# Optimization experiments

Hardware: AMD Instinct MI355X
Metric: run time of the kernel (lower is better)

Reference implementation:

```python
import jax, jax.numpy as jnp
import numpy as np

N = 10000      # nodes
E = 320000     # edges (avg degree 32)
C = 256        # feature dim (input_dim == output_dim)
L = 3          # num_layers
D = 20         # KAF dictionary size
BOUNDARY = 4.0 # KAF dictionary boundary


def setup_inputs() -> dict:
    key = jax.random.key(0)
    ks = jax.random.split(key, 7)
    x = jax.random.normal(ks[0], (N, C), jnp.float32)
    edge_index = jax.random.randint(ks[1], (2, E), 0, N, jnp.int32)
    edge_attr = jax.random.normal(ks[2], (E, 2), jnp.float32)
    # per-layer stacked parameters (all layers have identical shapes)
    node_w = jax.random.normal(ks[3], (L, C, C), jnp.float32) / jnp.sqrt(jnp.float32(C))
    edge_w = jax.random.normal(ks[4], (L, 2, C), jnp.float32) / jnp.sqrt(jnp.float32(2))
    neigh_w = jax.random.normal(ks[5], (L, C, C), jnp.float32) / jnp.sqrt(jnp.float32(C))
    bias = jnp.zeros((L, C), jnp.float32)
    alpha = jax.random.normal(ks[6], (L, C, D), jnp.float32) * 0.3
    return dict(x=x, edge_index=edge_index, edge_attr=edge_attr,
                node_w=node_w, edge_w=edge_w, neigh_w=neigh_w, bias=bias, alpha=alpha)


def _kaf(s, alpha_l):
    # Kernel Activation Function (Scardapane et al.): per-channel Gaussian mixture
    dict_pts = jnp.linspace(-BOUNDARY, BOUNDARY, D, dtype=s.dtype)  # [D]
    interval = 2.0 * BOUNDARY / (D - 1)
    gamma = 0.5 / (2.0 * interval) ** 2
    K = jnp.exp(-gamma * jnp.square(s[..., None] - dict_pts))  # [N, C, D]
    return jnp.einsum('ncd,cd->nc', K, alpha_l)


def reference(x, edge_index, edge_attr, node_w, edge_w, neigh_w, bias, alpha):
    src, dst = edge_index[0], edge_index[1]
    # mean-aggregation normalizer (computed once; graph is fixed across layers)
    cnt = jax.ops.segment_sum(jnp.ones((E,), x.dtype), dst, num_segments=N)
    inv_cnt = jnp.where(cnt > 0, 1.0 / jnp.maximum(cnt, 1.0), 0.0)  # [N]
    h = x
    for l in range(L):
        # message: edge_attr @ W_e + x_j @ W_n  -> [E, C]
        msg = edge_attr @ edge_w[l] + h[src] @ neigh_w[l]
        # mean aggregate to destination nodes
        aggr = jax.ops.segment_sum(msg, dst, num_segments=N) * inv_cnt[:, None]
        # update: KAF(aggr + x @ W + b)
        h = _kaf(aggr + h @ node_w[l] + bias[l], alpha[l])
    return h
```

## Files before the change

### kernel.cpp

```cpp
#include <hip/hip_runtime.h>
#include <hip/hip_bf16.h>

#define N_NODES 10000
#define N_EDGES 320000
#define CDIM    256
#define B_PRE   80
#define EPB     (N_EDGES / B_PRE)
#define SLK     258
#define SA      86

typedef __attribute__((ext_vector_type(8))) _Float16 half8;
typedef __attribute__((ext_vector_type(4))) _Float16 half4;
typedef __attribute__((ext_vector_type(4))) float floatx4;

#define OFF_RS    0
#define OFF_INVC  40960
#define OFF_S2    81920
#define OFF_COLV  163840
#define OFF_WCAT  806912
#define OFF_HN    1593344
#define OFF_HX    6713344
#define OFF_PERC  OFF_HN
#define OFF_BASE  (OFF_HN + 1600000)
#define OFF_EA2   OFF_HX
#define OFF_CTOT  (OFF_HX + 2560000)

__global__ __launch_bounds__(256) void k_prep(const float4* __restrict__ x, half4* __restrict__ hB,
                                              const float* __restrict__ neigh_w, const float* __restrict__ node_w,
                                              _Float16* __restrict__ wcatT) {
  __shared__ float t[32][33];
  const int b = blockIdx.x;
  if (b < 2500) {
    int i = b * 256 + threadIdx.x;
    float4 v = x[i];
    half4 h; h.x = (_Float16)v.x; h.y = (_Float16)v.y; h.z = (_Float16)v.z; h.w = (_Float16)v.w;
    hB[i] = h;
    return;
  }
  const int bb = b - 2500;
  const int k0 = (bb & 7) * 32;
  const int n0 = ((bb >> 3) & 15) * 32;
  const int l  = bb >> 7;
  const int tx = threadIdx.x & 31;
  const int ty = threadIdx.x >> 5;
  const float* src = (n0 < 256) ? neigh_w : node_w;
  const int nb = (n0 < 256) ? n0 : (n0 - 256);
#pragma unroll
  for (int p = 0; p < 4; ++p) {
    int k = k0 + ty + p * 8;
    t[ty + p * 8][tx] = src[l * 65536 + k * 256 + (nb + tx)];
  }
  __syncthreads();
#pragma unroll
  for (int p = 0; p < 4; ++p) {
    int n = n0 + ty + p * 8;
    wcatT[(size_t)l * 131072 + n * 256 + (k0 + tx)] = (_Float16)t[tx][ty + p * 8];
  }
}

__global__ __launch_bounds__(1024) void k_count(const int* __restrict__ ei,
                                                unsigned short* __restrict__ percnt) {
  __shared__ int hist[N_NODES];
  const int t = threadIdx.x, b = blockIdx.x;
  for (int n = t; n < N_NODES; n += 1024) hist[n] = 0;
  __syncthreads();
  const int e0 = b * EPB;
  for (int e = e0 + t; e < e0 + EPB; e += 1024)
    atomicAdd(&hist[ei[N_EDGES + e]], 1);
  __syncthreads();
  for (int n = t; n < N_NODES; n += 1024)
    percnt[b * N_NODES + n] = (unsigned short)hist[n];
}

__global__ __launch_bounds__(256) void k_base(const unsigned short* __restrict__ percnt,
                                              int* __restrict__ prefix, int* __restrict__ cnttot) {
  int n = blockIdx.x * 256 + threadIdx.x;
  if (n >= N_NODES) return;
  int s = 0;
  for (int b = 0; b < B_PRE; ++b) {
    prefix[b * N_NODES + n] = s;
    s += (int)percnt[b * N_NODES + n];
  }
  cnttot[n] = s;
}

__global__ __launch_bounds__(1024) void k_scan(const int* __restrict__ cnttot,
                                               int* __restrict__ rs, float* __restrict__ invc) {
  __shared__ int lds[1024];
  const int t = threadIdx.x;
  const int base = t * 10;
  int loc[10];
  int sum = 0;
#pragma unroll
  for (int i = 0; i < 10; ++i) {
    int idx = base + i;
    int v = (idx < N_NODES) ? cnttot[idx] : 0;
    loc[i] = v; sum += v;
  }
  lds[t] = sum; __syncthreads();
  for (int off = 1; off < 1024; off <<= 1) {
    int v = 0;
    if (t >= off) v = lds[t - off];
    __syncthreads();
    if (t >= off) lds[t] += v;
    __syncthreads();
  }
  int ex = lds[t] - sum;
#pragma unroll
  for (int i = 0; i < 10; ++i) {
    int idx = base + i;
    if (idx < N_NODES) {
      rs[idx] = ex; ex += loc[i];
      invc[idx] = (loc[i] > 0) ? (1.0f / (float)loc[i]) : 0.0f;
    }
  }
  if (t == 1023) rs[N_NODES] = lds[1023];
}

__global__ __launch_bounds__(1024) void k_scat(const int* __restrict__ ei, const float* __restrict__ ea,
                                               const int* __restrict__ prefix, const int* __restrict__ rs,
                                               unsigned short* __restrict__ colv, float2* __restrict__ ea2) {
  __shared__ int cur[N_NODES];
  const int t = threadIdx.x, b = blockIdx.x;
  for (int n = t; n < N_NODES; n += 1024)
    cur[n] = rs[n] + prefix[b * N_NODES + n];
  __syncthreads();
  const int e0 = b * EPB;
  for (int e = e0 + t; e < e0 + EPB; e += 1024) {
    int d = ei[N_EDGES + e];
    int src = ei[e];
    float2 a = ((const float2*)ea)[e];
    int pos = atomicAdd(&cur[d], 1);
    colv[pos] = (unsigned short)src;
    ea2[pos] = a;
  }
}

__global__ __launch_bounds__(256) void k_s2(const int* __restrict__ rs, const float2* __restrict__ ea2,
                                            float* __restrict__ s2) {
  int n = blockIdx.x * 256 + threadIdx.x;
  if (n >= N_NODES) return;
  int beg = rs[n], end = rs[n + 1];
  float sx = 0.f, sy = 0.f;
  for (int p = beg; p < end; ++p) { float2 a = ea2[p]; sx += a.x; sy += a.y; }
  s2[2 * n] = sx; s2[2 * n + 1] = sy;
}

__global__ __launch_bounds__(256) void k_gemm(const _Float16* __restrict__ A,
                                              const _Float16* __restrict__ BT,
                                              _Float16* __restrict__ hn,
                                              _Float16* __restrict__ hx) {
  __shared__ _Float16 As[64 * SLK];
  __shared__ _Float16 Bs[64 * SLK];
  const int tid = threadIdx.x;
  const int wv = tid >> 6;
  const int lane = tid & 63;
  const int m0 = blockIdx.x * 64;
  const int n0 = blockIdx.y * 64;
  const int wy = wv >> 1, wx = wv & 1;

  const int tr = tid >> 5;
  const int tc = (tid & 31) * 8;
  half8 av[8], bv[8];
#pragma unroll
  for (int s = 0; s < 8; ++s) {
    int arow = m0 + tr + 8 * s; if (arow >= N_NODES) arow = N_NODES - 1;
    av[s] = *(const half8*)(A + (size_t)arow * 256 + tc);
    bv[s] = *(const half8*)(BT + (size_t)(n0 + tr + 8 * s) * 256 + tc);
  }
#pragma unroll
  for (int s = 0; s < 8; ++s) {
    *(half8*)&As[(tr + 8 * s) * SLK + tc] = av[s];
    *(half8*)&Bs[(tr + 8 * s) * SLK + tc] = bv[s];
  }
  __syncthreads();

  floatx4 acc[2][2];
#pragma unroll
  for (int i = 0; i < 2; ++i)
#pragma unroll
    for (int j = 0; j < 2; ++j) acc[i][j] = (floatx4){0.f, 0.f, 0.f, 0.f};

  const int mrow = 32 * wy + (lane & 15);
  const int nrow = 32 * wx + (lane & 15);
  const int q8 = (lane >> 4) * 8;

#pragma unroll
  for (int kt = 0; kt < 8; ++kt) {
    const int kb = kt * 32 + q8;
    half8 af0 = *(const half8*)&As[mrow * SLK + kb];
    half8 af1 = *(const half8*)&As[(mrow + 16) * SLK + kb];
    half8 bf0 = *(const half8*)&Bs[nrow * SLK + kb];
    half8 bf1 = *(const half8*)&Bs[(nrow + 16) * SLK + kb];
    acc[0][0] = __builtin_amdgcn_mfma_f32_16x16x32_f16(af0, bf0, acc[0][0], 0, 0, 0);
    acc[0][1] = __builtin_amdgcn_mfma_f32_16x16x32_f16(af0, bf1, acc[0][1], 0, 0, 0);
    acc[1][0] = __builtin_amdgcn_mfma_f32_16x16x32_f16(af1, bf0, acc[1][0], 0, 0, 0);
    acc[1][1] = __builtin_amdgcn_mfma_f32_16x16x32_f16(af1, bf1, acc[1][1], 0, 0, 0);
  }

  const int colb = n0 + 32 * wx + (lane & 15);
  const int rowb = m0 + 32 * wy + 4 * (lane >> 4);
#pragma unroll
  for (int i = 0; i < 2; ++i) {
#pragma unroll
    for (int j = 0; j < 2; ++j) {
      const int cn = colb + 16 * j;
#pragma unroll
      for (int r = 0; r < 4; ++r) {
        const int rw = rowb + 16 * i + r;
        if (rw < N_NODES) {
          float v = acc[i][j][r];
          if (cn < 256) hn[rw * 256 + cn] = (_Float16)v;
          else          hx[rw * 256 + (cn - 256)] = (_Float16)v;
        }
      }
    }
  }
}

__global__ __launch_bounds__(256) void k_update(const int* __restrict__ rs, const unsigned short* __restrict__ colv,
                                                const float* __restrict__ invc, const float* __restrict__ s2,
                                                const _Float16* __restrict__ hn, const _Float16* __restrict__ hx,
                                                const float* __restrict__ ew,
                                                const float* __restrict__ bias,
                                                const float* __restrict__ alpha,
                                                _Float16* __restrict__ hmid, float* __restrict__ fout,
                                                int final_layer) {
  __shared__ float alds[64 * SA];
#pragma unroll
  for (int i = 0; i < 20; ++i) {
    int s = threadIdx.x + 256 * i;
    int c = s / 20, j = s - 20 * c;
    alds[(c >> 2) * SA + 4 * j + (c & 3)] = alpha[s];
  }
  __syncthreads();

  const int wv   = threadIdx.x >> 6;
  const int lane = threadIdx.x & 63;
  const int hf   = lane >> 5;
  const int l5   = lane & 31;
  const int n = blockIdx.x * 4 + wv;
  int beg = rs[n], end = rs[n + 1];
  beg = max(0, min(beg, N_EDGES));
  end = max(beg, min(end, N_EDGES));
  const int co = l5 * 8;

  half8 acc0 = (half8)(_Float16)0.f, acc1 = (half8)(_Float16)0.f;
  half8 acc2 = (half8)(_Float16)0.f, acc3 = (half8)(_Float16)0.f;
  for (int base = beg; base < end; base += 64) {
    const int cnt = min(64, end - base);
    int myIdx = 0;
    if (base + lane < end) myIdx = (int)colv[base + lane];
    int j = 0;
    for (; j + 8 <= cnt; j += 8) {
      int s0 = __shfl(myIdx, j + hf);
      int s1 = __shfl(myIdx, j + 2 + hf);
      int s2i = __shfl(myIdx, j + 4 + hf);
      int s3 = __shfl(myIdx, j + 6 + hf);
      half8 v0 = *(const half8*)(hn + (size_t)s0 * 256 + co);
      half8 v1 = *(const half8*)(hn + (size_t)s1 * 256 + co);
      half8 v2 = *(const half8*)(hn + (size_t)s2i * 256 + co);
      half8 v3 = *(const half8*)(hn + (size_t)s3 * 256 + co);
      acc0 += v0; acc1 += v1; acc2 += v2; acc3 += v3;
    }
    for (; j + 2 <= cnt; j += 2) {
      int s0 = __shfl(myIdx, j + hf);
      acc0 += *(const half8*)(hn + (size_t)s0 * 256 + co);
    }
    if (j < cnt) {
      int s0 = __shfl(myIdx, j);
      if (hf == 0)
        acc0 += *(const half8*)(hn + (size_t)s0 * 256 + co);
    }
  }
  acc0 = (acc0 + acc2) + (acc1 + acc3);
  union { half8 h; unsigned int u[4]; } me, ot;
  me.h = acc0;
#pragma unroll
  for (int r = 0; r < 4; ++r) ot.u[r] = (unsigned int)__shfl_xor((int)me.u[r], 32);
  acc0 = me.h + ot.h;

  const int c0 = l5 * 8 + hf * 4;
  float a0, a1, a2, a3;
  if (hf) { a0 = (float)acc0[4]; a1 = (float)acc0[5]; a2 = (float)acc0[6]; a3 = (float)acc0[7]; }
  else    { a0 = (float)acc0[0]; a1 = (float)acc0[1]; a2 = (float)acc0[2]; a3 = (float)acc0[3]; }

  const int q = c0 >> 2;
  const float ic = invc[n];
  const float t0 = s2[2 * n], t1 = s2[2 * n + 1];
  const half4  hv = ((const half4*)hx)[n * 64 + q];
  const float4 e0 = ((const float4*)ew)[q];
  const float4 e1 = ((const float4*)ew)[64 + q];
  const float4 bi = ((const float4*)bias)[q];
  float s[4];
  s[0] = (a0 + t0 * e0.x + t1 * e1.x) * ic + (float)hv.x + bi.x;
  s[1] = (a1 + t0 * e0.y + t1 * e1.y) * ic + (float)hv.y + bi.y;
  s[2] = (a2 + t0 * e0.z + t1 * e1.z) * ic + (float)hv.z + bi.z;
  s[3] = (a3 + t0 * e0.w + t1 * e1.w) * ic + (float)hv.w + bi.w;

  const float G = -0.705078125f;
  const float dp = 8.0f / 19.0f;
  const float* ar = &alds[q * SA];
  float o0 = 0.f, o1 = 0.f, o2 = 0.f, o3 = 0.f;
#pragma unroll
  for (int j = 0; j < 20; ++j) {
    float2 a01 = *(const float2*)(ar + 4 * j);
    float2 a23 = *(const float2*)(ar + 4 * j + 2);
    const float p = -4.0f + dp * (float)j;
    float x0 = s[0] - p, x1 = s[1] - p, x2 = s[2] - p, x3 = s[3] - p;
    o0 += a01.x * __expf(G * x0 * x0);
    o1 += a01.y * __expf(G * x1 * x1);
    o2 += a23.x * __expf(G * x2 * x2);
    o3 += a23.y * __expf(G * x3 * x3);
  }
  if (final_layer) {
    float4 w; w.x = o0; w.y = o1; w.z = o2; w.w = o3;
    ((float4*)fout)[n * 64 + q] = w;
  } else {
    half4 w; w.x = (_Float16)o0; w.y = (_Float16)o1; w.z = (_Float16)o2; w.w = (_Float16)o3;
    ((half4*)hmid)[n * 64 + q] = w;
  }
}

extern "C" void kernel_launch(void* const* d_in, const int* in_sizes, int n_in,
                              void* d_out, int out_size, void* d_ws, size_t ws_size,
                              hipStream_t stream) {
  const float* x       = (const float*)d_in[0];
  const int*   ei      = (const int*)d_in[1];
  const float* ea      = (const float*)d_in[2];
  const float* node_w  = (const float*)d_in[3];
  const float* edge_w  = (const float*)d_in[4];
  const float* neigh_w = (const float*)d_in[5];
  const float* bias    = (const float*)d_in[6];
  const float* alpha   = (const float*)d_in[7];

  char* w = (char*)d_ws;
  int*            rs     = (int*)(w + OFF_RS);
  float*          invc   = (float*)(w + OFF_INVC);
  float*          s2     = (float*)(w + OFF_S2);
  unsigned short* colv   = (unsigned short*)(w + OFF_COLV);
  _Float16*       wcatT  = (_Float16*)(w + OFF_WCAT);
  _Float16*       hn     = (_Float16*)(w + OFF_HN);
  _Float16*       hx     = (_Float16*)(w + OFF_HX);
  unsigned short* percnt = (unsigned short*)(w + OFF_PERC);
  int*            prefix = (int*)(w + OFF_BASE);
  float2*         ea2    = (float2*)(w + OFF_EA2);
  int*            cnttot = (int*)(w + OFF_CTOT);
  float*          fout   = (float*)d_out;
  _Float16*       hB     = (_Float16*)d_out;

  k_prep<<<2884, 256, 0, stream>>>((const float4*)x, (half4*)hB, neigh_w, node_w, wcatT);
  k_count<<<B_PRE, 1024, 0, stream>>>(ei, percnt);
  k_base<<<40, 256, 0, stream>>>(percnt, prefix, cnttot);
  k_scan<<<1, 1024, 0, stream>>>(cnttot, rs, invc);
  k_scat<<<B_PRE, 1024, 0, stream>>>(ei, ea, prefix, rs, colv, ea2);
  k_s2<<<40, 256, 0, stream>>>(rs, ea2, s2);

  for (int l = 0; l < 3; ++l) {
    k_gemm<<<dim3(157, 8, 1), 256, 0, stream>>>(hB, wcatT + l * 131072, hn, hx);
    k_update<<<2500, 256, 0, stream>>>(rs, colv, invc, s2, hn, hx,
                                       edge_w + l * 512, bias + l * 256, alpha + l * 5120,
                                       hB, fout, (l == 2) ? 1 : 0);
  }
}
```

Measured before the change: 238.7 us.

## Split update kernel channels into four 64-wide slices per block

The aggregation/KAF update kernel now launches four blocks per node group, each handling a 64-channel slice. Within a wave, 8 lanes cover the slice while 8 edge groups gather in parallel, followed by a shuffle reduction and an LDS bounce so each lane runs the KAF for a single channel. The goal is more parallelism and fewer KAF exps per thread. The cost is redundant index loads and block setup across slices, plus extra reduction shuffles. The LDS bounce relies on waitcnt with no barrier, which is within-wave only and so plausibly fine.

```diff
diff --git a/kernel.cpp b/kernel.cpp
--- a/kernel.cpp
+++ b/kernel.cpp
@@ -7,7 +7,6 @@
 #define B_PRE   80
 #define EPB     (N_EDGES / B_PRE)
 #define SLK     258
-#define SA      86
 
 typedef __attribute__((ext_vector_type(8))) _Float16 half8;
 typedef __attribute__((ext_vector_type(4))) _Float16 half4;
@@ -226,100 +225,84 @@
                                                 const float* __restrict__ alpha,
                                                 _Float16* __restrict__ hmid, float* __restrict__ fout,
                                                 int final_layer) {
-  __shared__ float alds[64 * SA];
-#pragma unroll
-  for (int i = 0; i < 20; ++i) {
+  __shared__ float aldsA[64 * 21];
+  __shared__ _Float16 bounce[4 * 64];
+  const int sl = blockIdx.x & 3;
+  const int nb = blockIdx.x >> 2;
+  const int co = sl * 64;
+
+#pragma unroll
+  for (int i = 0; i < 5; ++i) {
     int s = threadIdx.x + 256 * i;
     int c = s / 20, j = s - 20 * c;
-    alds[(c >> 2) * SA + 4 * j + (c & 3)] = alpha[s];
+    aldsA[c * 21 + j] = alpha[co * 20 + s];
   }
   __syncthreads();
 
   const int wv   = threadIdx.x >> 6;
   const int lane = threadIdx.x & 63;
-  const int hf   = lane >> 5;
-  const int l5   = lane & 31;
-  const int n = blockIdx.x * 4 + wv;
+  const int g    = lane >> 3;
+  const int li   = lane & 7;
+  const int n = nb * 4 + wv;
   int beg = rs[n], end = rs[n + 1];
   beg = max(0, min(beg, N_EDGES));
   end = max(beg, min(end, N_EDGES));
-  const int co = l5 * 8;
+  const _Float16* hsl = hn + co + li * 8;
 
   half8 acc0 = (half8)(_Float16)0.f, acc1 = (half8)(_Float16)0.f;
   half8 acc2 = (half8)(_Float16)0.f, acc3 = (half8)(_Float16)0.f;
+  const half8 zero = (half8)(_Float16)0.f;
   for (int base = beg; base < end; base += 64) {
     const int cnt = min(64, end - base);
     int myIdx = 0;
     if (base + lane < end) myIdx = (int)colv[base + lane];
     int j = 0;
-    for (; j + 8 <= cnt; j += 8) {
-      int s0 = __shfl(myIdx, j + hf);
-      int s1 = __shfl(myIdx, j + 2 + hf);
-      int s2i = __shfl(myIdx, j + 4 + hf);
-      int s3 = __shfl(myIdx, j + 6 + hf);
-      half8 v0 = *(const half8*)(hn + (size_t)s0 * 256 + co);
-      half8 v1 = *(const half8*)(hn + (size_t)s1 * 256 + co);
-      half8 v2 = *(const half8*)(hn + (size_t)s2i * 256 + co);
-      half8 v3 = *(const half8*)(hn + (size_t)s3 * 256 + co);
-      acc0 += v0; acc1 += v1; acc2 += v2; acc3 += v3;
+    for (; j + 32 <= cnt; j += 32) {
+      int s0 = __shfl(myIdx, j + g);
+      int s1 = __shfl(myIdx, j + 8 + g);
+      int s2i = __shfl(myIdx, j + 16 + g);
+      int s3 = __shfl(myIdx, j + 24 + g);
+      acc0 += *(const half8*)(hsl + (size_t)s0 * 256);
+      acc1 += *(const half8*)(hsl + (size_t)s1 * 256);
+      acc2 += *(const half8*)(hsl + (size_t)s2i * 256);
+      acc3 += *(const half8*)(hsl + (size_t)s3 * 256);
     }
-    for (; j + 2 <= cnt; j += 2) {
-      int s0 = __shfl(myIdx, j + hf);
-      acc0 += *(const half8*)(hn + (size_t)s0 * 256 + co);
-    }
-    if (j < cnt) {
-      int s0 = __shfl(myIdx, j);
-      if (hf == 0)
-        acc0 += *(const half8*)(hn + (size_t)s0 * 256 + co);
+    for (; j < cnt; j += 8) {
+      int e = j + g;
+      int s0 = __shfl(myIdx, (e < 64) ? e : 0);
+      half8 v = (e < cnt) ? *(const half8*)(hsl + (size_t)s0 * 256) : zero;
+      acc0 += v;
     }
   }
   acc0 = (acc0 + acc2) + (acc1 + acc3);
   union { half8 h; unsigned int u[4]; } me, ot;
-  me.h = acc0;
-#pragma unroll
-  for (int r = 0; r < 4; ++r) ot.u[r] = (unsigned int)__shfl_xor((int)me.u[r], 32);
-  acc0 = me.h + ot.h;
-
-  const int c0 = l5 * 8 + hf * 4;
-  float a0, a1, a2, a3;
-  if (hf) { a0 = (float)acc0[4]; a1 = (float)acc0[5]; a2 = (float)acc0[6]; a3 = (float)acc0[7]; }
-  else    { a0 = (float)acc0[0]; a1 = (float)acc0[1]; a2 = (float)acc0[2]; a3 = (float)acc0[3]; }
-
-  const int q = c0 >> 2;
+#pragma unroll
+  for (int m = 8; m <= 32; m <<= 1) {
+    me.h = acc0;
+#pragma unroll
+    for (int r = 0; r < 4; ++r) ot.u[r] = (unsigned int)__shfl_xor((int)me.u[r], m);
+    acc0 = me.h + ot.h;
+  }
+  if (g == 0) *(half8*)&bounce[wv * 64 + li * 8] = acc0;
+  __builtin_amdgcn_s_waitcnt(0);
+  float a = (float)bounce[wv * 64 + lane];
+
+  const int ch = co + lane;
   const float ic = invc[n];
   const float t0 = s2[2 * n], t1 = s2[2 * n + 1];
-  const half4  hv = ((const half4*)hx)[n * 64 + q];
-  const float4 e0 = ((const float4*)ew)[q];
-  const float4 e1 = ((const float4*)ew)[64 + q];
-  const float4 bi = ((const float4*)bias)[q];
-  float s[4];
-  s[0] = (a0 + t0 * e0.x + t1 * e1.x) * ic + (float)hv.x + bi.x;
-  s[1] = (a1 + t0 * e0.y + t1 * e1.y) * ic + (float)hv.y + bi.y;
-  s[2] = (a2 + t0 * e0.z + t1 * e1.z) * ic + (float)hv.z + bi.z;
-  s[3] = (a3 + t0 * e0.w + t1 * e1.w) * ic + (float)hv.w + bi.w;
+  const float sv = (a + t0 * ew[ch] + t1 * ew[256 + ch]) * ic + (float)hx[n * 256 + ch] + bias[ch];
 
   const float G = -0.705078125f;
   const float dp = 8.0f / 19.0f;
-  const float* ar = &alds[q * SA];
-  float o0 = 0.f, o1 = 0.f, o2 = 0.f, o3 = 0.f;
+  const float* ar = &aldsA[lane * 21];
+  float ov = 0.f;
 #pragma unroll
   for (int j = 0; j < 20; ++j) {
-    float2 a01 = *(const float2*)(ar + 4 * j);
-    float2 a23 = *(const float2*)(ar + 4 * j + 2);
-    const float p = -4.0f + dp * (float)j;
-    float x0 = s[0] - p, x1 = s[1] - p, x2 = s[2] - p, x3 = s[3] - p;
-    o0 += a01.x * __expf(G * x0 * x0);
-    o1 += a01.y * __expf(G * x1 * x1);
-    o2 += a23.x * __expf(G * x2 * x2);
-    o3 += a23.y * __expf(G * x3 * x3);
-  }
-  if (final_layer) {
-    float4 w; w.x = o0; w.y = o1; w.z = o2; w.w = o3;
-    ((float4*)fout)[n * 64 + q] = w;
-  } else {
-    half4 w; w.x = (_Float16)o0; w.y = (_Float16)o1; w.z = (_Float16)o2; w.w = (_Float16)o3;
-    ((half4*)hmid)[n * 64 + q] = w;
-  }
+    float xj = sv - (-4.0f + dp * (float)j);
+    ov += ar[j] * __expf(G * xj * xj);
+  }
+  if (final_layer) fout[n * 256 + ch] = ov;
+  else             hmid[n * 256 + ch] = (_Float16)ov;
 }
 
 extern "C" void kernel_launch(void* const* d_in, const int* in_sizes, int n_in,
@@ -358,8 +341,8 @@
 
   for (int l = 0; l < 3; ++l) {
     k_gemm<<<dim3(157, 8, 1), 256, 0, stream>>>(hB, wcatT + l * 131072, hn, hx);
-    k_update<<<2500, 256, 0, stream>>>(rs, colv, invc, s2, hn, hx,
-                                       edge_w + l * 512, bias + l * 256, alpha + l * 5120,
-                                       hB, fout, (l == 2) ? 1 : 0);
-  }
-}
+    k_update<<<10000, 256, 0, stream>>>(rs, colv, invc, s2, hn, hx,
+                                        edge_w + l * 512, bias + l * 256, alpha + l * 5120,
+                                        hB, fout, (l == 2) ? 1 : 0);
+  }
+}
```

Result: slower. 245.1 us (+2.7%).
